# Kernel tuning notes

Measured on AMD Instinct MI355X. Metric: run time of the kernel, lower is better.

## Reference

```python
import jax, jax.numpy as jnp
import numpy as np

B, H, W = 16, 288, 384
NUM_ITER = 5      # LMSolver num_iter
LM_DAMP = 1e-4
Z_MIN = 0.01      # PerspectiveCamera z_min
REL_DELTA = 0.1   # AdaptiveHuberPnPCost relative_delta


def skew(v):
    x, y, z = v[..., 0], v[..., 1], v[..., 2]
    O = jnp.zeros_like(x)
    return jnp.stack([jnp.stack([O, -z, y], -1),
                      jnp.stack([z, O, -x], -1),
                      jnp.stack([-y, x, O], -1)], -2)


def exp_so3(w):
    th = jnp.maximum(jnp.linalg.norm(w, axis=-1, keepdims=True), 1e-8)
    K = skew(w / th)
    th = th[..., None]
    I = jnp.eye(3, dtype=w.dtype)
    return I + jnp.sin(th) * K + (1.0 - jnp.cos(th)) * (K @ K)


def se3_inv(T):
    R = T[..., :3, :3]
    t = T[..., :3, 3]
    Rt = jnp.swapaxes(R, -1, -2)
    ti = -jnp.einsum('...ij,...j->...i', Rt, t)
    return (jnp.zeros_like(T).at[..., :3, :3].set(Rt)
            .at[..., :3, 3].set(ti).at[..., 3, 3].set(1.0))


def project(x3d, R, t, K):
    Xc = jnp.einsum('bij,bnj->bni', R, x3d) + t[:, None]  # [B,N,3]
    z = jnp.maximum(Xc[..., 2], Z_MIN)
    fx, fy = K[:, 0, 0, None], K[:, 1, 1, None]
    cx, cy = K[:, 0, 2, None], K[:, 1, 2, None]
    uv = jnp.stack([fx * Xc[..., 0] / z + cx, fy * Xc[..., 1] / z + cy], -1)
    return uv, Xc


def lm_pnp(x3d, x2d, w2d, K):
    """Batched robust Levenberg-Marquardt PnP (replaces per-sample Python loop)."""
    Bb = x3d.shape[0]
    dt = x3d.dtype
    # AdaptiveHuberPnPCost.set_param: delta from spread of x2d
    delta = REL_DELTA * jnp.sqrt(jnp.var(x2d, axis=1).sum(-1))  # [B]
    R = jnp.broadcast_to(jnp.eye(3, dtype=dt), (Bb, 3, 3))
    t = jnp.zeros((Bb, 3), dt)
    I6 = jnp.eye(6, dtype=dt)
    for _ in range(NUM_ITER):
        uv, Xc = project(x3d, R, t, K)
        r = uv - x2d                           # [B,N,2]
        wr = w2d * r
        rn = jnp.linalg.norm(wr, axis=-1)      # [B,N]
        rob = jnp.sqrt(jnp.minimum(1.0, delta[:, None] / jnp.maximum(rn, 1e-8)))
        wt = w2d * rob[..., None]              # [B,N,2] Huber-IRLS weights
        z = jnp.maximum(Xc[..., 2], Z_MIN)
        iz = 1.0 / z
        fx, fy = K[:, 0, 0, None], K[:, 1, 1, None]
        zero = jnp.zeros_like(iz)
        Jp = jnp.stack([
            jnp.stack([fx * iz, zero, -fx * Xc[..., 0] * iz * iz], -1),
            jnp.stack([zero, fy * iz, -fy * Xc[..., 1] * iz * iz], -1)], -2)  # [B,N,2,3]
        Jrot = -jnp.einsum('bnij,bnjk->bnik', Jp, skew(Xc))
        J = jnp.concatenate([Jp, Jrot], -1)    # [B,N,2,6]
        Jw = J * wt[..., None]
        JTJ = jnp.einsum('bnif,bnig->bfg', Jw, Jw)
        JTr = jnp.einsum('bnif,bni->bf', Jw, wt * r)
        damp = LM_DAMP * jnp.trace(JTJ, axis1=-2, axis2=-1)[:, None, None] / 6.0 + 1e-6
        dx = -jnp.linalg.solve(JTJ + damp * I6, JTr[..., None])[..., 0]
        t = t + dx[:, :3]
        R = exp_so3(dx[:, 3:]) @ R
    T = (jnp.zeros((Bb, 4, 4), dt).at[:, :3, :3].set(R)
         .at[:, :3, 3].set(t).at[:, 3, 3].set(1.0))
    return T


def setup_inputs() -> dict:
    key = jax.random.key(0)
    k1, k2, k3, k4, k5 = jax.random.split(key, 5)
    f = 350.0
    Kmat = jnp.array([[f, 0.0, W / 2.0], [0.0, f, H / 2.0], [0.0, 0.0, 1.0]], jnp.float32)
    K = jnp.broadcast_to(Kmat, (B, 3, 3))
    # geometrically consistent points: backproject pixel grid with random depth
    xs = jnp.arange(W, dtype=jnp.float32)
    ys = jnp.arange(H, dtype=jnp.float32)
    gx, gy = jnp.meshgrid(xs, ys, indexing='xy')          # [H,W]
    depth = 2.0 + 4.0 * jax.random.uniform(k1, (B, H, W))
    X = (gx - W / 2.0) / f * depth
    Y = (gy - H / 2.0) / f * depth
    pts3d = jnp.stack([X, Y, depth], -1)
    pts3d = pts3d + 0.02 * jax.random.normal(k2, pts3d.shape)
    conf = 1.0 + jax.random.uniform(k3, (B, H, W))
    # valid SE(3) gt poses (small perturbations of identity)
    q = jax.random.normal(k4, (B, 4)) * 0.05
    q = q.at[:, 0].add(1.0)
    q = q / jnp.linalg.norm(q, axis=-1, keepdims=True)
    w_, x_, y_, z_ = q[:, 0], q[:, 1], q[:, 2], q[:, 3]
    Rg = jnp.stack([
        jnp.stack([1 - 2 * (y_**2 + z_**2), 2 * (x_ * y_ - z_ * w_), 2 * (x_ * z_ + y_ * w_)], -1),
        jnp.stack([2 * (x_ * y_ + z_ * w_), 1 - 2 * (x_**2 + z_**2), 2 * (y_ * z_ - x_ * w_)], -1),
        jnp.stack([2 * (x_ * z_ - y_ * w_), 2 * (y_ * z_ + x_ * w_), 1 - 2 * (x_**2 + y_**2)], -1)], -2)
    tg = 0.2 * jax.random.normal(k5, (B, 3))
    pose = (jnp.zeros((B, 4, 4), jnp.float32).at[:, :3, :3].set(Rg)
            .at[:, :3, 3].set(tg).at[:, 3, 3].set(1.0))
    return {'pts3d_in_other_view': pts3d.astype(jnp.float32),
            'conf': conf.astype(jnp.float32),
            'camera_intrinsics': K.astype(jnp.float32),
            'camera_pose': pose}


def reference(pts3d_in_other_view, conf, camera_intrinsics, camera_pose):
    Bb, Hh, Ww, _ = pts3d_in_other_view.shape
    N = Hh * Ww
    xs = jnp.arange(Ww, dtype=pts3d_in_other_view.dtype)
    ys = jnp.arange(Hh, dtype=pts3d_in_other_view.dtype)
    gx, gy = jnp.meshgrid(xs, ys, indexing='xy')
    pixels = jnp.stack([gx, gy], -1).reshape(1, N, 2)
    x3d = pts3d_in_other_view.reshape(Bb, N, 3)
    x2d = jnp.broadcast_to(pixels, (Bb, N, 2))
    w2d = jnp.broadcast_to(conf.reshape(Bb, N, 1), (Bb, N, 2))
    pred_poses = lm_pnp(x3d, x2d, w2d, camera_intrinsics)
    gt_rel = jnp.einsum('ij,bjk->bik', se3_inv(camera_pose[0]), camera_pose)
    pred_rel = jnp.einsum('ij,bjk->bik', se3_inv(pred_poses[0]), pred_poses)
    R_gt, R_pr = gt_rel[:, :3, :3], pred_rel[:, :3, :3]
    t_gt, t_pr = gt_rel[:, :3, 3], pred_rel[:, :3, 3]
    Rd = jnp.einsum('bji,bjk->bik', R_pr, R_gt)
    trace = Rd[:, 0, 0] + Rd[:, 1, 1] + Rd[:, 2, 2]
    cosang = jnp.clip(0.5 * (trace - 1.0), -1.0 + 1e-7, 1.0 - 1e-7)
    rot_loss = jnp.arccos(cosang).mean()
    trans_loss = jnp.linalg.norm(t_pr - t_gt, axis=-1).mean()
    return rot_loss + trans_loss, rot_loss, trans_loss
```

## Files before the change

### kernel.cpp

```cpp
#include <hip/hip_runtime.h>
#include <math.h>

#define NB 16
#define IMH 288
#define IMW 384
#define NPIX (IMH*IMW)
#define TPB 256
#define PPT 8
#define BPB (NPIX/(TPB*PPT))
#define NBLK (NB*BPB)
#define NITER 5

#define POSE_OFF 0
#define ACC_OFF (2*NB*12)
#define WS_DOUBLES (2*NB*12 + NITER*NB*27)

__device__ __forceinline__ void solve_update(const double* __restrict__ acc,
                                             const double* __restrict__ pin,
                                             double* __restrict__ Ro,
                                             double* __restrict__ to) {
    double A[6][6], rhs[6], inv[6];
    {
        int k = 0;
        #pragma unroll
        for (int f = 0; f < 6; f++) {
            #pragma unroll 6
            for (int g = f; g < 6; g++) {
                double v = acc[k];
                A[f][g] = v; A[g][f] = v; k++;
            }
        }
    }
    #pragma unroll
    for (int f = 0; f < 6; f++) rhs[f] = -acc[21 + f];

    double tr = A[0][0] + A[1][1] + A[2][2] + A[3][3] + A[4][4] + A[5][5];
    double damp = 1e-4 * tr / 6.0 + 1e-6;
    #pragma unroll
    for (int f = 0; f < 6; f++) A[f][f] += damp;

    #pragma unroll
    for (int j = 0; j < 6; j++) {
        double s = A[j][j];
        #pragma unroll 6
        for (int m = 0; m < j; m++) s -= A[j][m] * A[j][m];
        double dd = sqrt(fmax(s, 1e-30));
        A[j][j] = dd;
        inv[j] = 1.0 / dd;
        #pragma unroll 6
        for (int i = j + 1; i < 6; i++) {
            double s2 = A[i][j];
            #pragma unroll 6
            for (int m = 0; m < j; m++) s2 -= A[i][m] * A[j][m];
            A[i][j] = s2 * inv[j];
        }
    }
    #pragma unroll
    for (int i = 0; i < 6; i++) {
        double s = rhs[i];
        #pragma unroll 6
        for (int m = 0; m < i; m++) s -= A[i][m] * rhs[m];
        rhs[i] = s * inv[i];
    }
    #pragma unroll
    for (int i = 5; i >= 0; i--) {
        double s = rhs[i];
        #pragma unroll 6
        for (int m = i + 1; m < 6; m++) s -= A[m][i] * rhs[m];
        rhs[i] = s * inv[i];
    }

    to[0] = pin[9]  + rhs[0];
    to[1] = pin[10] + rhs[1];
    to[2] = pin[11] + rhs[2];

    double wx = rhs[3], wy = rhs[4], wz = rhs[5];
    double th = sqrt(wx*wx + wy*wy + wz*wz);
    th = fmax(th, 1e-8);
    double ith = 1.0 / th;
    double kx = wx*ith, ky = wy*ith, kz = wz*ith;
    float stf, ctf;
    sincosf((float)th, &stf, &ctf);
    double st = (double)stf, ct = 1.0 - (double)ctf;
    double E[9];
    E[0] = 1.0 + ct*(kx*kx - 1.0);
    E[1] = -st*kz + ct*kx*ky;
    E[2] =  st*ky + ct*kx*kz;
    E[3] =  st*kz + ct*ky*kx;
    E[4] = 1.0 + ct*(ky*ky - 1.0);
    E[5] = -st*kx + ct*ky*kz;
    E[6] = -st*ky + ct*kz*kx;
    E[7] =  st*kx + ct*kz*ky;
    E[8] = 1.0 + ct*(kz*kz - 1.0);

    #pragma unroll
    for (int i = 0; i < 3; i++) {
        #pragma unroll
        for (int j = 0; j < 3; j++)
            Ro[i*3+j] = E[i*3+0]*pin[0*3+j] + E[i*3+1]*pin[1*3+j] + E[i*3+2]*pin[2*3+j];
    }
}

__global__ void init_k(double* ws) {
    int i = threadIdx.x;
    for (int k = i; k < WS_DOUBLES; k += TPB) ws[k] = 0.0;
    __syncthreads();
    if (i < NB) {
        double* p = ws + POSE_OFF + i * 12;
        p[0] = 1.0; p[4] = 1.0; p[8] = 1.0;
    }
}

__global__ __launch_bounds__(TPB) void reduce_k(const float* __restrict__ x3d,
                                                const float* __restrict__ conf,
                                                const float* __restrict__ Kmat,
                                                double* __restrict__ ws, int it) {
    const int b = blockIdx.x / BPB;
    const int chunk = blockIdx.x % BPB;

    __shared__ double sp[12];
    __shared__ double lds[TPB / 64][27];

    float R[9], t[3];
    if (it == 0) {
        R[0]=1.f; R[1]=0.f; R[2]=0.f;
        R[3]=0.f; R[4]=1.f; R[5]=0.f;
        R[6]=0.f; R[7]=0.f; R[8]=1.f;
        t[0]=t[1]=t[2]=0.f;
    } else {
        if ((threadIdx.x >> 6) == 0) {
            const double* accp = ws + ACC_OFF + ((size_t)(it-1) * NB + b) * 27;
            const double* pin  = ws + POSE_OFF + (size_t)((it-1) & 1) * NB * 12 + b * 12;
            double Rn[9], tn[3];
            solve_update(accp, pin, Rn, tn);
            if (threadIdx.x == 0) {
                #pragma unroll
                for (int i = 0; i < 9; i++) sp[i] = Rn[i];
                sp[9] = tn[0]; sp[10] = tn[1]; sp[11] = tn[2];
                if (chunk == 0) {
                    double* pout = ws + POSE_OFF + (size_t)(it & 1) * NB * 12 + b * 12;
                    #pragma unroll
                    for (int i = 0; i < 9; i++) pout[i] = Rn[i];
                    pout[9] = tn[0]; pout[10] = tn[1]; pout[11] = tn[2];
                }
            }
        }
        __syncthreads();
        #pragma unroll
        for (int i = 0; i < 9; i++) R[i] = (float)sp[i];
        t[0] = (float)sp[9]; t[1] = (float)sp[10]; t[2] = (float)sp[11];
    }

    const float fx = Kmat[b*9 + 0];
    const float fy = Kmat[b*9 + 4];
    const float cx = Kmat[b*9 + 2];
    const float cy = Kmat[b*9 + 5];
    const float delta = (float)(0.1 * sqrt(((double)(IMW*IMW - 1) + (double)(IMH*IMH - 1)) / 12.0));

    float facc[27];
    #pragma unroll
    for (int i = 0; i < 27; i++) facc[i] = 0.0f;

    const int ft = chunk * TPB + threadIdx.x;
    const int n0 = ft * PPT;
    const int v0 = n0 / IMW;
    const float cyv  = cy - (float)v0;
    const float cxu0 = cx - (float)(n0 - v0 * IMW);

    const float4* P4 = reinterpret_cast<const float4*>(x3d + (size_t)b * NPIX * 3) + (size_t)ft * 6;
    const float4* W4 = reinterpret_cast<const float4*>(conf + (size_t)b * NPIX) + (size_t)ft * 2;

    #pragma unroll
    for (int grp = 0; grp < 2; ++grp) {
        const float4 va = P4[grp*3 + 0];
        const float4 vb = P4[grp*3 + 1];
        const float4 vc = P4[grp*3 + 2];
        const float4 vw = W4[grp];
        float ppx[4] = { va.x, va.w, vb.z, vc.y };
        float ppy[4] = { va.y, vb.x, vb.w, vc.z };
        float ppz[4] = { va.z, vb.y, vc.x, vc.w };
        float pw[4]  = { vw.x, vw.y, vw.z, vw.w };

        #pragma unroll
        for (int g = 0; g < 4; ++g) {
            float px = ppx[g], py = ppy[g], pz = ppz[g], w = pw[g];
            float u_off = cxu0 - (float)(grp * 4 + g);

            float Xx = fmaf(R[0], px, fmaf(R[1], py, fmaf(R[2], pz, t[0])));
            float Xy = fmaf(R[3], px, fmaf(R[4], py, fmaf(R[5], pz, t[1])));
            float Xz = fmaf(R[6], px, fmaf(R[7], py, fmaf(R[8], pz, t[2])));
            float z  = fmaxf(Xz, 0.01f);
            float iz = __builtin_amdgcn_rcpf(z);

            float Xxiz = Xx * iz, Xyiz = Xy * iz;
            float rx = fmaf(fx, Xxiz, u_off);
            float ry = fmaf(fy, Xyiz, cyv);

            float wrx = w * rx, wry = w * ry;
            float q  = fmaf(wrx, wrx, wry * wry);
            float rs = __builtin_amdgcn_rsqf(fmaxf(q, 1e-16f));
            float rob2 = fminf(1.0f, delta * rs);
            float sq = w * __builtin_amdgcn_sqrtf(rob2);

            float sqiz = sq * iz;
            float a  = fx * sqiz;
            float c  = fy * sqiz;
            float bb = -a * Xxiz;
            float d  = -c * Xyiz;

            float j0[6] = { a, 0.0f, bb,  bb*Xy,               fmaf(a, Xz, -bb*Xx), -a*Xy };
            float j1[6] = { 0.0f, c,  d,  fmaf(d, Xy, -c*Xz), -d*Xx,                 c*Xx };
            float rxs = sq * rx, rys = sq * ry;

            int k = 0;
            #pragma unroll
            for (int f = 0; f < 6; ++f) {
                #pragma unroll
                for (int gg = f; gg < 6; ++gg) {
                    facc[k] += j0[f]*j0[gg] + j1[f]*j1[gg];
                    k++;
                }
            }
            #pragma unroll
            for (int f = 0; f < 6; ++f)
                facc[21 + f] += j0[f]*rxs + j1[f]*rys;
        }
    }

    int lane = threadIdx.x & 63;
    int wave = threadIdx.x >> 6;
    #pragma unroll
    for (int i = 0; i < 27; i++) {
        float v = facc[i];
        for (int off = 32; off > 0; off >>= 1) v += __shfl_down(v, off, 64);
        if (lane == 0) lds[wave][i] = (double)v;
    }
    __syncthreads();

    double* acc = ws + ACC_OFF + ((size_t)it * NB + b) * 27;
    if (threadIdx.x < 27) {
        double v = 0.0;
        #pragma unroll
        for (int wv = 0; wv < TPB/64; wv++) v += lds[wv][threadIdx.x];
        atomicAdd(acc + threadIdx.x, v);
    }
}

__global__ __launch_bounds__(64) void loss_k(const double* __restrict__ ws,
                                             const float* __restrict__ pose,
                                             float* __restrict__ out) {
    int lane = threadIdx.x;
    double Rp[9] = {1,0,0, 0,1,0, 0,0,1}, tp[3] = {0,0,0};
    if (lane < NB) {
        const double* accp = ws + ACC_OFF + ((size_t)(NITER-1) * NB + lane) * 27;
        const double* pin  = ws + POSE_OFF + (size_t)((NITER-1) & 1) * NB * 12 + lane * 12;
        solve_update(accp, pin, Rp, tp);
    }
    double Rp0[9], tp0v[3];
    #pragma unroll
    for (int i = 0; i < 9; i++) Rp0[i] = __shfl(Rp[i], 0, 64);
    #pragma unroll
    for (int i = 0; i < 3; i++) tp0v[i] = __shfl(tp[i], 0, 64);

    double rot = 0.0, trans = 0.0;
    if (lane < NB) {
        const float* P0 = pose;
        const float* Pb = pose + lane * 16;
        double R0t[9];
        #pragma unroll
        for (int i = 0; i < 3; i++)
            #pragma unroll
            for (int j = 0; j < 3; j++) R0t[i*3+j] = (double)P0[j*4+i];
        double t0i[3];
        #pragma unroll
        for (int i = 0; i < 3; i++)
            t0i[i] = -(R0t[i*3+0]*P0[0*4+3] + R0t[i*3+1]*P0[1*4+3] + R0t[i*3+2]*P0[2*4+3]);
        double Rg[9], tg[3];
        #pragma unroll
        for (int i = 0; i < 3; i++) {
            #pragma unroll
            for (int j = 0; j < 3; j++)
                Rg[i*3+j] = R0t[i*3+0]*Pb[0*4+j] + R0t[i*3+1]*Pb[1*4+j] + R0t[i*3+2]*Pb[2*4+j];
            tg[i] = R0t[i*3+0]*Pb[0*4+3] + R0t[i*3+1]*Pb[1*4+3] + R0t[i*3+2]*Pb[2*4+3] + t0i[i];
        }
        double Rp0t[9];
        #pragma unroll
        for (int i = 0; i < 3; i++)
            #pragma unroll
            for (int j = 0; j < 3; j++) Rp0t[i*3+j] = Rp0[j*3+i];
        double tp0i[3];
        #pragma unroll
        for (int i = 0; i < 3; i++)
            tp0i[i] = -(Rp0t[i*3+0]*tp0v[0] + Rp0t[i*3+1]*tp0v[1] + Rp0t[i*3+2]*tp0v[2]);
        double Rr[9], tr[3];
        #pragma unroll
        for (int i = 0; i < 3; i++) {
            #pragma unroll
            for (int j = 0; j < 3; j++)
                Rr[i*3+j] = Rp0t[i*3+0]*Rp[0*3+j] + Rp0t[i*3+1]*Rp[1*3+j] + Rp0t[i*3+2]*Rp[2*3+j];
            tr[i] = Rp0t[i*3+0]*tp[0] + Rp0t[i*3+1]*tp[1] + Rp0t[i*3+2]*tp[2] + tp0i[i];
        }
        double trace = 0.0;
        #pragma unroll
        for (int i = 0; i < 3; i++)
            trace += Rr[0*3+i]*Rg[0*3+i] + Rr[1*3+i]*Rg[1*3+i] + Rr[2*3+i]*Rg[2*3+i];
        double cosang = 0.5 * (trace - 1.0);
        double lo = -1.0 + 1e-7, hi = 1.0 - 1e-7;
        cosang = fmin(fmax(cosang, lo), hi);
        rot = acos(cosang);
        double d0 = tr[0]-tg[0], d1 = tr[1]-tg[1], d2 = tr[2]-tg[2];
        trans = sqrt(d0*d0 + d1*d1 + d2*d2);
    }
    for (int off = 8; off > 0; off >>= 1) {
        rot   += __shfl_down(rot, off, 64);
        trans += __shfl_down(trans, off, 64);
    }
    if (lane == 0) {
        rot /= NB; trans /= NB;
        out[0] = (float)(rot + trans);
        out[1] = (float)rot;
        out[2] = (float)trans;
    }
}

extern "C" void kernel_launch(void* const* d_in, const int* in_sizes, int n_in,
                              void* d_out, int out_size, void* d_ws, size_t ws_size,
                              hipStream_t stream) {
    const float* x3d  = (const float*)d_in[0];
    const float* conf = (const float*)d_in[1];
    const float* Kmat = (const float*)d_in[2];
    const float* pose = (const float*)d_in[3];
    float* out = (float*)d_out;
    double* ws = (double*)d_ws;

    hipLaunchKernelGGL(init_k, dim3(1), dim3(TPB), 0, stream, ws);
    for (int it = 0; it < NITER; ++it) {
        hipLaunchKernelGGL(reduce_k, dim3(NBLK), dim3(TPB), 0, stream,
                           x3d, conf, Kmat, ws, it);
    }
    hipLaunchKernelGGL(loss_k, dim3(1), dim3(64), 0, stream, ws, pose, out);
}
```

Measured before the change: 86.02 us.

## Fuse loss into last reduce pass, use packed FMAs and transpose-shuffle reduction

Removes the separate loss kernel. The last reduce pass now uses per-image and global atomic counters so the final block solves the last LM update and then computes the loss. The per-pixel normal-equation accumulation switches to packed two-wide float FMAs. The 27 per-wave sums are reduced with a recursive-halving butterfly over 32 lanes instead of 27 independent shuffle trees. All global loads are also hoisted ahead of the pose-solve step so their latency overlaps it. The cost is a more complex last-block synchronisation, which relies on threadfence and atomics for correctness.

```diff
diff --git a/kernel.cpp b/kernel.cpp
--- a/kernel.cpp
+++ b/kernel.cpp
@@ -11,30 +11,33 @@
 #define NBLK (NB*BPB)
 #define NITER 5
 
+typedef float v2f __attribute__((ext_vector_type(2)));
+
 #define POSE_OFF 0
-#define ACC_OFF (2*NB*12)
-#define WS_DOUBLES (2*NB*12 + NITER*NB*27)
-
-__device__ __forceinline__ void solve_update(const double* __restrict__ acc,
-                                             const double* __restrict__ pin,
-                                             double* __restrict__ Ro,
-                                             double* __restrict__ to) {
+#define PFIN_OFF (2*NB*12)
+#define ACC_OFF  (2*NB*12 + NB*12)
+#define WS_DOUBLES (ACC_OFF + NITER*NB*27)
+
+__device__ __forceinline__ v2f sp2(float x){ v2f r; r[0]=x; r[1]=x; return r; }
+__device__ __forceinline__ v2f pkfma(v2f a, float b, v2f c){ return __builtin_elementwise_fma(a, sp2(b), c); }
+
+__device__ __forceinline__ void solve_update(const double* acc, const double* pin,
+                                             double* Ro, double* to) {
     double A[6][6], rhs[6], inv[6];
     {
         int k = 0;
         #pragma unroll
-        for (int f = 0; f < 6; f++) {
+        for (int f = 0; f < 6; f++)
             #pragma unroll 6
             for (int g = f; g < 6; g++) {
                 double v = acc[k];
                 A[f][g] = v; A[g][f] = v; k++;
             }
-        }
     }
     #pragma unroll
     for (int f = 0; f < 6; f++) rhs[f] = -acc[21 + f];
 
-    double tr = A[0][0] + A[1][1] + A[2][2] + A[3][3] + A[4][4] + A[5][5];
+    double tr = A[0][0]+A[1][1]+A[2][2]+A[3][3]+A[4][4]+A[5][5];
     double damp = 1e-4 * tr / 6.0 + 1e-6;
     #pragma unroll
     for (int f = 0; f < 6; f++) A[f][f] += damp;
@@ -43,7 +46,7 @@
     for (int j = 0; j < 6; j++) {
         double s = A[j][j];
         #pragma unroll 6
-        for (int m = 0; m < j; m++) s -= A[j][m] * A[j][m];
+        for (int m = 0; m < j; m++) s -= A[j][m]*A[j][m];
         double dd = sqrt(fmax(s, 1e-30));
         A[j][j] = dd;
         inv[j] = 1.0 / dd;
@@ -51,7 +54,7 @@
         for (int i = j + 1; i < 6; i++) {
             double s2 = A[i][j];
             #pragma unroll 6
-            for (int m = 0; m < j; m++) s2 -= A[i][m] * A[j][m];
+            for (int m = 0; m < j; m++) s2 -= A[i][m]*A[j][m];
             A[i][j] = s2 * inv[j];
         }
     }
@@ -59,14 +62,14 @@
     for (int i = 0; i < 6; i++) {
         double s = rhs[i];
         #pragma unroll 6
-        for (int m = 0; m < i; m++) s -= A[i][m] * rhs[m];
+        for (int m = 0; m < i; m++) s -= A[i][m]*rhs[m];
         rhs[i] = s * inv[i];
     }
     #pragma unroll
     for (int i = 5; i >= 0; i--) {
         double s = rhs[i];
         #pragma unroll 6
-        for (int m = i + 1; m < 6; m++) s -= A[m][i] * rhs[m];
+        for (int m = i + 1; m < 6; m++) s -= A[m][i]*rhs[m];
         rhs[i] = s * inv[i];
     }
 
@@ -75,8 +78,7 @@
     to[2] = pin[11] + rhs[2];
 
     double wx = rhs[3], wy = rhs[4], wz = rhs[5];
-    double th = sqrt(wx*wx + wy*wy + wz*wz);
-    th = fmax(th, 1e-8);
+    double th = fmax(sqrt(wx*wx + wy*wy + wz*wz), 1e-8);
     double ith = 1.0 / th;
     double kx = wx*ith, ky = wy*ith, kz = wz*ith;
     float stf, ctf;
@@ -94,16 +96,81 @@
     E[8] = 1.0 + ct*(kz*kz - 1.0);
 
     #pragma unroll
-    for (int i = 0; i < 3; i++) {
+    for (int i = 0; i < 3; i++)
         #pragma unroll
         for (int j = 0; j < 3; j++)
             Ro[i*3+j] = E[i*3+0]*pin[0*3+j] + E[i*3+1]*pin[1*3+j] + E[i*3+2]*pin[2*3+j];
+}
+
+__device__ __forceinline__ void loss_dev(const double* ws, const float* pose, float* out) {
+    int lane = threadIdx.x;
+    double rot = 0.0, trans = 0.0;
+    const double* pf0 = ws + PFIN_OFF;
+    if (lane < NB) {
+        const float* P0 = pose;
+        const float* Pb = pose + lane * 16;
+        double R0t[9];
+        #pragma unroll
+        for (int i = 0; i < 3; i++)
+            #pragma unroll
+            for (int j = 0; j < 3; j++) R0t[i*3+j] = (double)P0[j*4+i];
+        double t0i[3];
+        #pragma unroll
+        for (int i = 0; i < 3; i++)
+            t0i[i] = -(R0t[i*3+0]*P0[0*4+3] + R0t[i*3+1]*P0[1*4+3] + R0t[i*3+2]*P0[2*4+3]);
+        double Rg[9], tg[3];
+        #pragma unroll
+        for (int i = 0; i < 3; i++) {
+            #pragma unroll
+            for (int j = 0; j < 3; j++)
+                Rg[i*3+j] = R0t[i*3+0]*Pb[0*4+j] + R0t[i*3+1]*Pb[1*4+j] + R0t[i*3+2]*Pb[2*4+j];
+            tg[i] = R0t[i*3+0]*Pb[0*4+3] + R0t[i*3+1]*Pb[1*4+3] + R0t[i*3+2]*Pb[2*4+3] + t0i[i];
+        }
+        const double* pfb = ws + PFIN_OFF + lane * 12;
+        double Rp0t[9];
+        #pragma unroll
+        for (int i = 0; i < 3; i++)
+            #pragma unroll
+            for (int j = 0; j < 3; j++) Rp0t[i*3+j] = pf0[j*3+i];
+        double tp0i[3];
+        #pragma unroll
+        for (int i = 0; i < 3; i++)
+            tp0i[i] = -(Rp0t[i*3+0]*pf0[9] + Rp0t[i*3+1]*pf0[10] + Rp0t[i*3+2]*pf0[11]);
+        double Rr[9], trv[3];
+        #pragma unroll
+        for (int i = 0; i < 3; i++) {
+            #pragma unroll
+            for (int j = 0; j < 3; j++)
+                Rr[i*3+j] = Rp0t[i*3+0]*pfb[0*3+j] + Rp0t[i*3+1]*pfb[1*3+j] + Rp0t[i*3+2]*pfb[2*3+j];
+            trv[i] = Rp0t[i*3+0]*pfb[9] + Rp0t[i*3+1]*pfb[10] + Rp0t[i*3+2]*pfb[11] + tp0i[i];
+        }
+        double trace = 0.0;
+        #pragma unroll
+        for (int i = 0; i < 3; i++)
+            trace += Rr[0*3+i]*Rg[0*3+i] + Rr[1*3+i]*Rg[1*3+i] + Rr[2*3+i]*Rg[2*3+i];
+        double cosang = 0.5 * (trace - 1.0);
+        cosang = fmin(fmax(cosang, -1.0 + 1e-7), 1.0 - 1e-7);
+        rot = acos(cosang);
+        double d0 = trv[0]-tg[0], d1 = trv[1]-tg[1], d2 = trv[2]-tg[2];
+        trans = sqrt(d0*d0 + d1*d1 + d2*d2);
+    }
+    for (int off = 8; off > 0; off >>= 1) {
+        rot   += __shfl_down(rot, off, 64);
+        trans += __shfl_down(trans, off, 64);
+    }
+    if (lane == 0) {
+        rot /= NB; trans /= NB;
+        out[0] = (float)(rot + trans);
+        out[1] = (float)rot;
+        out[2] = (float)trans;
     }
 }
 
 __global__ void init_k(double* ws) {
     int i = threadIdx.x;
     for (int k = i; k < WS_DOUBLES; k += TPB) ws[k] = 0.0;
+    int* cnt = (int*)(ws + WS_DOUBLES);
+    for (int k = i; k < NB + 1; k += TPB) cnt[k] = 0;
     __syncthreads();
     if (i < NB) {
         double* p = ws + POSE_OFF + i * 12;
@@ -114,12 +181,22 @@
 __global__ __launch_bounds__(TPB) void reduce_k(const float* __restrict__ x3d,
                                                 const float* __restrict__ conf,
                                                 const float* __restrict__ Kmat,
-                                                double* __restrict__ ws, int it) {
+                                                const float* __restrict__ pose,
+                                                float* __restrict__ out,
+                                                double* __restrict__ ws,
+                                                int it, int last) {
     const int b = blockIdx.x / BPB;
     const int chunk = blockIdx.x % BPB;
-
-    __shared__ double sp[12];
-    __shared__ double lds[TPB / 64][27];
+    const int tid = threadIdx.x;
+
+    const int ft = chunk * TPB + tid;
+    const float4* P4 = reinterpret_cast<const float4*>(x3d + (size_t)b * NPIX * 3) + (size_t)ft * 6;
+    const float4* W4 = reinterpret_cast<const float4*>(conf + (size_t)b * NPIX) + (size_t)ft * 2;
+    const float4 va = P4[0], vb = P4[1], vc = P4[2], vd = P4[3], ve = P4[4], vf = P4[5];
+    const float4 w0 = W4[0], w1 = W4[1];
+
+    __shared__ double sps[12];
+    __shared__ double lred[4][27];
 
     float R[9], t[3];
     if (it == 0) {
@@ -128,17 +205,17 @@
         R[6]=0.f; R[7]=0.f; R[8]=1.f;
         t[0]=t[1]=t[2]=0.f;
     } else {
-        if ((threadIdx.x >> 6) == 0) {
-            const double* accp = ws + ACC_OFF + ((size_t)(it-1) * NB + b) * 27;
-            const double* pin  = ws + POSE_OFF + (size_t)((it-1) & 1) * NB * 12 + b * 12;
+        if (tid < 64) {
             double Rn[9], tn[3];
-            solve_update(accp, pin, Rn, tn);
-            if (threadIdx.x == 0) {
+            solve_update(ws + ACC_OFF + ((size_t)(it-1) * NB + b) * 27,
+                         ws + POSE_OFF + (size_t)((it-1) & 1) * NB * 12 + (size_t)b * 12,
+                         Rn, tn);
+            if (tid == 0) {
                 #pragma unroll
-                for (int i = 0; i < 9; i++) sp[i] = Rn[i];
-                sp[9] = tn[0]; sp[10] = tn[1]; sp[11] = tn[2];
+                for (int i = 0; i < 9; i++) sps[i] = Rn[i];
+                sps[9] = tn[0]; sps[10] = tn[1]; sps[11] = tn[2];
                 if (chunk == 0) {
-                    double* pout = ws + POSE_OFF + (size_t)(it & 1) * NB * 12 + b * 12;
+                    double* pout = ws + POSE_OFF + (size_t)(it & 1) * NB * 12 + (size_t)b * 12;
                     #pragma unroll
                     for (int i = 0; i < 9; i++) pout[i] = Rn[i];
                     pout[9] = tn[0]; pout[10] = tn[1]; pout[11] = tn[2];
@@ -147,8 +224,8 @@
         }
         __syncthreads();
         #pragma unroll
-        for (int i = 0; i < 9; i++) R[i] = (float)sp[i];
-        t[0] = (float)sp[9]; t[1] = (float)sp[10]; t[2] = (float)sp[11];
+        for (int i = 0; i < 9; i++) R[i] = (float)sps[i];
+        t[0] = (float)sps[9]; t[1] = (float)sps[10]; t[2] = (float)sps[11];
     }
 
     const float fx = Kmat[b*9 + 0];
@@ -157,169 +234,134 @@
     const float cy = Kmat[b*9 + 5];
     const float delta = (float)(0.1 * sqrt(((double)(IMW*IMW - 1) + (double)(IMH*IMH - 1)) / 12.0));
 
-    float facc[27];
-    #pragma unroll
-    for (int i = 0; i < 27; i++) facc[i] = 0.0f;
-
-    const int ft = chunk * TPB + threadIdx.x;
     const int n0 = ft * PPT;
     const int v0 = n0 / IMW;
     const float cyv  = cy - (float)v0;
     const float cxu0 = cx - (float)(n0 - v0 * IMW);
 
-    const float4* P4 = reinterpret_cast<const float4*>(x3d + (size_t)b * NPIX * 3) + (size_t)ft * 6;
-    const float4* W4 = reinterpret_cast<const float4*>(conf + (size_t)b * NPIX) + (size_t)ft * 2;
-
-    #pragma unroll
-    for (int grp = 0; grp < 2; ++grp) {
-        const float4 va = P4[grp*3 + 0];
-        const float4 vb = P4[grp*3 + 1];
-        const float4 vc = P4[grp*3 + 2];
-        const float4 vw = W4[grp];
-        float ppx[4] = { va.x, va.w, vb.z, vc.y };
-        float ppy[4] = { va.y, vb.x, vb.w, vc.z };
-        float ppz[4] = { va.z, vb.y, vc.x, vc.w };
-        float pw[4]  = { vw.x, vw.y, vw.z, vw.w };
-
-        #pragma unroll
-        for (int g = 0; g < 4; ++g) {
-            float px = ppx[g], py = ppy[g], pz = ppz[g], w = pw[g];
-            float u_off = cxu0 - (float)(grp * 4 + g);
-
-            float Xx = fmaf(R[0], px, fmaf(R[1], py, fmaf(R[2], pz, t[0])));
-            float Xy = fmaf(R[3], px, fmaf(R[4], py, fmaf(R[5], pz, t[1])));
-            float Xz = fmaf(R[6], px, fmaf(R[7], py, fmaf(R[8], pz, t[2])));
-            float z  = fmaxf(Xz, 0.01f);
-            float iz = __builtin_amdgcn_rcpf(z);
-
-            float Xxiz = Xx * iz, Xyiz = Xy * iz;
-            float rx = fmaf(fx, Xxiz, u_off);
-            float ry = fmaf(fy, Xyiz, cyv);
-
-            float wrx = w * rx, wry = w * ry;
-            float q  = fmaf(wrx, wrx, wry * wry);
-            float rs = __builtin_amdgcn_rsqf(fmaxf(q, 1e-16f));
-            float rob2 = fminf(1.0f, delta * rs);
-            float sq = w * __builtin_amdgcn_sqrtf(rob2);
-
-            float sqiz = sq * iz;
-            float a  = fx * sqiz;
-            float c  = fy * sqiz;
-            float bb = -a * Xxiz;
-            float d  = -c * Xyiz;
-
-            float j0[6] = { a, 0.0f, bb,  bb*Xy,               fmaf(a, Xz, -bb*Xx), -a*Xy };
-            float j1[6] = { 0.0f, c,  d,  fmaf(d, Xy, -c*Xz), -d*Xx,                 c*Xx };
-            float rxs = sq * rx, rys = sq * ry;
-
-            int k = 0;
-            #pragma unroll
-            for (int f = 0; f < 6; ++f) {
+    float ppx[8] = { va.x, va.w, vb.z, vc.y, vd.x, vd.w, ve.z, vf.y };
+    float ppy[8] = { va.y, vb.x, vb.w, vc.z, vd.y, ve.x, ve.w, vf.z };
+    float ppz[8] = { va.z, vb.y, vc.x, vc.w, vd.z, ve.y, vf.x, vf.w };
+    float pw[8]  = { w0.x, w0.y, w0.z, w0.w, w1.x, w1.y, w1.z, w1.w };
+
+    v2f A0[3], A1[3], A2[2], A3[2], A4, A5, AR[3];
+    #pragma unroll
+    for (int i = 0; i < 3; i++) { A0[i]=sp2(0.f); A1[i]=sp2(0.f); AR[i]=sp2(0.f); }
+    A2[0]=sp2(0.f); A2[1]=sp2(0.f); A3[0]=sp2(0.f); A3[1]=sp2(0.f);
+    A4=sp2(0.f); A5=sp2(0.f);
+
+    #pragma unroll
+    for (int g = 0; g < PPT; ++g) {
+        float px = ppx[g], py = ppy[g], pz = ppz[g], w = pw[g];
+
+        float Xx = fmaf(R[0], px, fmaf(R[1], py, fmaf(R[2], pz, t[0])));
+        float Xy = fmaf(R[3], px, fmaf(R[4], py, fmaf(R[5], pz, t[1])));
+        float Xz = fmaf(R[6], px, fmaf(R[7], py, fmaf(R[8], pz, t[2])));
+        float z  = fmaxf(Xz, 0.01f);
+        float iz = __builtin_amdgcn_rcpf(z);
+
+        float Xxiz = Xx * iz, Xyiz = Xy * iz;
+        float rx = fmaf(fx, Xxiz, cxu0 - (float)g);
+        float ry = fmaf(fy, Xyiz, cyv);
+
+        float wrx = w * rx, wry = w * ry;
+        float q  = fmaf(wrx, wrx, wry * wry);
+        float rs = __builtin_amdgcn_rsqf(fmaxf(q, 1e-16f));
+        float rob2 = fminf(1.0f, delta * rs);
+        float sq = w * __builtin_amdgcn_sqrtf(rob2);
+
+        float sqiz = sq * iz;
+        float a  = fx * sqiz;
+        float c  = fy * sqiz;
+        float bb = -a * Xxiz;
+        float d  = -c * Xyiz;
+
+        float j03 = bb * Xy;
+        float j04 = fmaf(a, Xz, -bb * Xx);
+        float j05 = -a * Xy;
+        float j13 = fmaf(d, Xy, -c * Xz);
+        float j14 = -d * Xx;
+        float j15 = c * Xx;
+        float rxs = sq * rx, rys = sq * ry;
+
+        v2f j0p0; j0p0[0]=a;   j0p0[1]=0.f;
+        v2f j0p1; j0p1[0]=bb;  j0p1[1]=j03;
+        v2f j0p2; j0p2[0]=j04; j0p2[1]=j05;
+        v2f j1p0; j1p0[0]=0.f; j1p0[1]=c;
+        v2f j1p1; j1p1[0]=d;   j1p1[1]=j13;
+        v2f j1p2; j1p2[0]=j14; j1p2[1]=j15;
+
+        A0[0]=pkfma(j0p0,a,A0[0]);  A0[1]=pkfma(j0p1,a,A0[1]);  A0[2]=pkfma(j0p2,a,A0[2]);
+        A1[0]=pkfma(j1p0,c,A1[0]);  A1[1]=pkfma(j1p1,c,A1[1]);  A1[2]=pkfma(j1p2,c,A1[2]);
+        A2[0]=pkfma(j0p1,bb,A2[0]); A2[0]=pkfma(j1p1,d,A2[0]);
+        A2[1]=pkfma(j0p2,bb,A2[1]); A2[1]=pkfma(j1p2,d,A2[1]);
+        A3[0]=pkfma(j0p1,j03,A3[0]); A3[0]=pkfma(j1p1,j13,A3[0]);
+        A3[1]=pkfma(j0p2,j03,A3[1]); A3[1]=pkfma(j1p2,j13,A3[1]);
+        A4 = pkfma(j0p2,j04,A4);     A4 = pkfma(j1p2,j14,A4);
+        A5 = pkfma(j0p2,j05,A5);     A5 = pkfma(j1p2,j15,A5);
+        AR[0]=pkfma(j0p0,rxs,AR[0]); AR[0]=pkfma(j1p0,rys,AR[0]);
+        AR[1]=pkfma(j0p1,rxs,AR[1]); AR[1]=pkfma(j1p1,rys,AR[1]);
+        AR[2]=pkfma(j0p2,rxs,AR[2]); AR[2]=pkfma(j1p2,rys,AR[2]);
+    }
+
+    float cur[32];
+    cur[0]=A0[0][0];  cur[1]=A0[0][1];  cur[2]=A0[1][0];  cur[3]=A0[1][1];  cur[4]=A0[2][0];  cur[5]=A0[2][1];
+    cur[6]=A1[0][1];  cur[7]=A1[1][0];  cur[8]=A1[1][1];  cur[9]=A1[2][0];  cur[10]=A1[2][1];
+    cur[11]=A2[0][0]; cur[12]=A2[0][1]; cur[13]=A2[1][0]; cur[14]=A2[1][1];
+    cur[15]=A3[0][1]; cur[16]=A3[1][0]; cur[17]=A3[1][1];
+    cur[18]=A4[0];    cur[19]=A4[1];
+    cur[20]=A5[1];
+    cur[21]=AR[0][0]; cur[22]=AR[0][1]; cur[23]=AR[1][0]; cur[24]=AR[1][1]; cur[25]=AR[2][0]; cur[26]=AR[2][1];
+    cur[27]=0.f; cur[28]=0.f; cur[29]=0.f; cur[30]=0.f; cur[31]=0.f;
+
+    const int lane = tid & 63;
+    const int wave = tid >> 6;
+    #pragma unroll
+    for (int s = 0; s < 5; ++s) {
+        const int m = 1 << s;
+        const int h = 16 >> s;
+        const bool up = (lane & m) != 0;
+        #pragma unroll
+        for (int i = 0; i < h; ++i) {
+            float keep = up ? cur[i + h] : cur[i];
+            float send = up ? cur[i]     : cur[i + h];
+            cur[i] = keep + __shfl_xor(send, m, 64);
+        }
+    }
+    float tot = cur[0] + __shfl_xor(cur[0], 32, 64);
+    int vidx = __brev((unsigned)lane) >> 27;
+    if (lane < 32 && vidx < 27) lred[wave][vidx] = (double)tot;
+    __syncthreads();
+
+    double* acc = ws + ACC_OFF + ((size_t)it * NB + b) * 27;
+    if (tid < 27)
+        atomicAdd(acc + tid, lred[0][tid] + lred[1][tid] + lred[2][tid] + lred[3][tid]);
+
+    if (last) {
+        __shared__ int s_doloss;
+        __syncthreads();
+        if (tid == 0) {
+            s_doloss = 0;
+            int* cnt = (int*)(ws + WS_DOUBLES);
+            int old = atomicAdd(&cnt[b], 1);
+            if (old == BPB - 1) {
+                __threadfence();
+                double Rn[9], tn[3];
+                solve_update(acc, sps, Rn, tn);
+                double* pf = ws + PFIN_OFF + (size_t)b * 12;
                 #pragma unroll
-                for (int gg = f; gg < 6; ++gg) {
-                    facc[k] += j0[f]*j0[gg] + j1[f]*j1[gg];
-                    k++;
-                }
+                for (int i = 0; i < 9; i++) pf[i] = Rn[i];
+                pf[9] = tn[0]; pf[10] = tn[1]; pf[11] = tn[2];
+                __threadfence();
+                int o2 = atomicAdd(&cnt[NB], 1);
+                if (o2 == NB - 1) s_doloss = 1;
             }
-            #pragma unroll
-            for (int f = 0; f < 6; ++f)
-                facc[21 + f] += j0[f]*rxs + j1[f]*rys;
-        }
-    }
-
-    int lane = threadIdx.x & 63;
-    int wave = threadIdx.x >> 6;
-    #pragma unroll
-    for (int i = 0; i < 27; i++) {
-        float v = facc[i];
-        for (int off = 32; off > 0; off >>= 1) v += __shfl_down(v, off, 64);
-        if (lane == 0) lds[wave][i] = (double)v;
-    }
-    __syncthreads();
-
-    double* acc = ws + ACC_OFF + ((size_t)it * NB + b) * 27;
-    if (threadIdx.x < 27) {
-        double v = 0.0;
-        #pragma unroll
-        for (int wv = 0; wv < TPB/64; wv++) v += lds[wv][threadIdx.x];
-        atomicAdd(acc + threadIdx.x, v);
-    }
-}
-
-__global__ __launch_bounds__(64) void loss_k(const double* __restrict__ ws,
-                                             const float* __restrict__ pose,
-                                             float* __restrict__ out) {
-    int lane = threadIdx.x;
-    double Rp[9] = {1,0,0, 0,1,0, 0,0,1}, tp[3] = {0,0,0};
-    if (lane < NB) {
-        const double* accp = ws + ACC_OFF + ((size_t)(NITER-1) * NB + lane) * 27;
-        const double* pin  = ws + POSE_OFF + (size_t)((NITER-1) & 1) * NB * 12 + lane * 12;
-        solve_update(accp, pin, Rp, tp);
-    }
-    double Rp0[9], tp0v[3];
-    #pragma unroll
-    for (int i = 0; i < 9; i++) Rp0[i] = __shfl(Rp[i], 0, 64);
-    #pragma unroll
-    for (int i = 0; i < 3; i++) tp0v[i] = __shfl(tp[i], 0, 64);
-
-    double rot = 0.0, trans = 0.0;
-    if (lane < NB) {
-        const float* P0 = pose;
-        const float* Pb = pose + lane * 16;
-        double R0t[9];
-        #pragma unroll
-        for (int i = 0; i < 3; i++)
-            #pragma unroll
-            for (int j = 0; j < 3; j++) R0t[i*3+j] = (double)P0[j*4+i];
-        double t0i[3];
-        #pragma unroll
-        for (int i = 0; i < 3; i++)
-            t0i[i] = -(R0t[i*3+0]*P0[0*4+3] + R0t[i*3+1]*P0[1*4+3] + R0t[i*3+2]*P0[2*4+3]);
-        double Rg[9], tg[3];
-        #pragma unroll
-        for (int i = 0; i < 3; i++) {
-            #pragma unroll
-            for (int j = 0; j < 3; j++)
-                Rg[i*3+j] = R0t[i*3+0]*Pb[0*4+j] + R0t[i*3+1]*Pb[1*4+j] + R0t[i*3+2]*Pb[2*4+j];
-            tg[i] = R0t[i*3+0]*Pb[0*4+3] + R0t[i*3+1]*Pb[1*4+3] + R0t[i*3+2]*Pb[2*4+3] + t0i[i];
-        }
-        double Rp0t[9];
-        #pragma unroll
-        for (int i = 0; i < 3; i++)
-            #pragma unroll
-            for (int j = 0; j < 3; j++) Rp0t[i*3+j] = Rp0[j*3+i];
-        double tp0i[3];
-        #pragma unroll
-        for (int i = 0; i < 3; i++)
-            tp0i[i] = -(Rp0t[i*3+0]*tp0v[0] + Rp0t[i*3+1]*tp0v[1] + Rp0t[i*3+2]*tp0v[2]);
-        double Rr[9], tr[3];
-        #pragma unroll
-        for (int i = 0; i < 3; i++) {
-            #pragma unroll
-            for (int j = 0; j < 3; j++)
-                Rr[i*3+j] = Rp0t[i*3+0]*Rp[0*3+j] + Rp0t[i*3+1]*Rp[1*3+j] + Rp0t[i*3+2]*Rp[2*3+j];
-            tr[i] = Rp0t[i*3+0]*tp[0] + Rp0t[i*3+1]*tp[1] + Rp0t[i*3+2]*tp[2] + tp0i[i];
-        }
-        double trace = 0.0;
-        #pragma unroll
-        for (int i = 0; i < 3; i++)
-            trace += Rr[0*3+i]*Rg[0*3+i] + Rr[1*3+i]*Rg[1*3+i] + Rr[2*3+i]*Rg[2*3+i];
-        double cosang = 0.5 * (trace - 1.0);
-        double lo = -1.0 + 1e-7, hi = 1.0 - 1e-7;
-        cosang = fmin(fmax(cosang, lo), hi);
-        rot = acos(cosang);
-        double d0 = tr[0]-tg[0], d1 = tr[1]-tg[1], d2 = tr[2]-tg[2];
-        trans = sqrt(d0*d0 + d1*d1 + d2*d2);
-    }
-    for (int off = 8; off > 0; off >>= 1) {
-        rot   += __shfl_down(rot, off, 64);
-        trans += __shfl_down(trans, off, 64);
-    }
-    if (lane == 0) {
-        rot /= NB; trans /= NB;
-        out[0] = (float)(rot + trans);
-        out[1] = (float)rot;
-        out[2] = (float)trans;
+        }
+        __syncthreads();
+        if (s_doloss && tid < 64) {
+            __threadfence();
+            loss_dev(ws, pose, out);
+        }
     }
 }
 
@@ -336,7 +378,6 @@
     hipLaunchKernelGGL(init_k, dim3(1), dim3(TPB), 0, stream, ws);
     for (int it = 0; it < NITER; ++it) {
         hipLaunchKernelGGL(reduce_k, dim3(NBLK), dim3(TPB), 0, stream,
-                           x3d, conf, Kmat, ws, it);
-    }
-    hipLaunchKernelGGL(loss_k, dim3(1), dim3(64), 0, stream, ws, pose, out);
-}
+                           x3d, conf, Kmat, pose, out, ws, it, (it == NITER - 1) ? 1 : 0);
+    }
+}
```

Result: slower. 191.4 us (+122.5%).
